# Performance work log

Measured on AMD Instinct MI355X. Metric: run time of the kernel, lower is better.

The kernel has to match this reference:

```python
import jax, jax.numpy as jnp
import numpy as np

B, C, H, W = 4, 64, 64, 64
K = C // 8  # conv_f / conv_g output channels (scale=8 since C>=8)


def setup_inputs() -> dict:
    key = jax.random.key(0)
    ks = jax.random.split(key, 8)
    x = jax.random.normal(ks[0], (B, C, H, W), dtype=jnp.float32)
    Wf = jax.random.normal(ks[1], (K, C), dtype=jnp.float32) * 0.05
    bf = jnp.zeros((K,), dtype=jnp.float32)
    Wg = jax.random.normal(ks[2], (K, C), dtype=jnp.float32) * 0.05
    bg = jnp.zeros((K,), dtype=jnp.float32)
    Wh = jax.random.normal(ks[3], (C, C), dtype=jnp.float32) * 0.05
    bh = jnp.zeros((C,), dtype=jnp.float32)
    gamma = jax.random.uniform(ks[4], (1,), dtype=jnp.float32)
    return {"x": x, "Wf": Wf, "bf": bf, "Wg": Wg, "bg": bg,
            "Wh": Wh, "bh": bh, "gamma": gamma}


def reference(x, Wf, bf, Wg, bg, Wh, bh, gamma):
    Bn, Cn, Hn, Wn = x.shape
    HW = Hn * Wn
    xf = x.reshape(Bn, Cn, HW)                               # [B, C, HW]
    # 1x1 convs == per-pixel linear maps over channels
    f = jnp.einsum('kc,bcn->bkn', Wf, xf) + bf[None, :, None]  # [B, K, HW]
    g = jnp.einsum('kc,bcn->bkn', Wg, xf) + bg[None, :, None]  # [B, K, HW]
    h = jnp.einsum('dc,bcn->bdn', Wh, xf) + bh[None, :, None]  # [B, C, HW]
    # s = f^T @ g  -> [B, HW, HW]
    s = jnp.einsum('bki,bkj->bij', f, g)
    # softmax over dim=1 (the first HW axis), matching F.softmax(s, dim=1)
    b = jax.nn.softmax(s, axis=1)
    # post-softmax lower-triangular mask applied to b^T (lower_tri=True)
    tri = jnp.tril(jnp.ones((HW, HW), dtype=x.dtype))
    b_masked = jnp.swapaxes(b, 1, 2) * tri                   # [B, HW, HW]
    o = jnp.einsum('bcn,bnm->bcm', h, b_masked)              # [B, C, HW]
    y = (gamma[0] * o + xf).reshape(Bn, Cn, Hn, Wn)
    return y
```

## Files before the change

### kernel.cpp

```cpp
#include <hip/hip_runtime.h>
#include <hip/hip_bf16.h>

#define HW 4096
#define CC 64
#define NB 4

typedef short bf16x8 __attribute__((ext_vector_type(8)));
typedef float f32x4 __attribute__((ext_vector_type(4)));

#define OFF_F  0
#define OFF_G  262144
#define OFF_H  524288
#define OFF_ZI 2621440
#define OFF_O  2686976

__device__ __forceinline__ float bf2f(short s) {
    unsigned u = ((unsigned)(unsigned short)s) << 16;
    return __uint_as_float(u);
}

__global__ __launch_bounds__(256) void k_prep(
    const float* __restrict__ x,
    const float* __restrict__ Wf, const float* __restrict__ bf,
    const float* __restrict__ Wg, const float* __restrict__ bg,
    const float* __restrict__ Wh, const float* __restrict__ bh,
    __hip_bfloat16* __restrict__ fb, __hip_bfloat16* __restrict__ gb,
    __hip_bfloat16* __restrict__ hb)
{
    __shared__ __align__(16) __hip_bfloat16 xT[64 * 72];
    __shared__ __align__(16) __hip_bfloat16 fgT[64 * 24];

    const int b  = blockIdx.y;
    const int n0 = blockIdx.x * 64;
    const int tid = (int)threadIdx.x;
    const int w = tid >> 6, lane = tid & 63, quad = lane >> 4, l15 = lane & 15;

    {
        const int n = lane;
        const float* xb = x + (size_t)b * (CC * HW) + n0 + n;
#pragma unroll
        for (int i = 0; i < 8; ++i) {
            const int c = (w + 4 * i) * 2;
            const float v0 = xb[(size_t)c * HW];
            const float v1 = xb[(size_t)(c + 1) * HW];
            __hip_bfloat16 t[2] = {__float2bfloat16(v0), __float2bfloat16(v1)};
            *reinterpret_cast<unsigned*>(&xT[n * 72 + c]) =
                *reinterpret_cast<const unsigned*>(t);
        }
    }

    bf16x8 wa[5][2];
#pragma unroll
    for (int mt = 0; mt < 5; ++mt) {
        const int row = mt * 16 + l15;
        const float* src = (row < 8) ? (Wf + row * 64)
                         : (row < 16) ? (Wg + (row - 8) * 64)
                                      : (Wh + (row - 16) * 64);
#pragma unroll
        for (int kk = 0; kk < 2; ++kk) {
            const float4 a = *(const float4*)(src + kk * 32 + quad * 8);
            const float4 c4 = *(const float4*)(src + kk * 32 + quad * 8 + 4);
            __hip_bfloat16 t[8];
            t[0] = __float2bfloat16(a.x);  t[1] = __float2bfloat16(a.y);
            t[2] = __float2bfloat16(a.z);  t[3] = __float2bfloat16(a.w);
            t[4] = __float2bfloat16(c4.x); t[5] = __float2bfloat16(c4.y);
            t[6] = __float2bfloat16(c4.z); t[7] = __float2bfloat16(c4.w);
            wa[mt][kk] = *reinterpret_cast<const bf16x8*>(t);
        }
    }

    f32x4 acc[5];
#pragma unroll
    for (int mt = 0; mt < 5; ++mt) {
#pragma unroll
        for (int r = 0; r < 4; ++r) {
            const int grow = mt * 16 + quad * 4 + r;
            acc[mt][r] = (grow < 8) ? bf[grow]
                       : (grow < 16) ? bg[grow - 8]
                                     : bh[grow - 16];
        }
    }

    __syncthreads();

    const bf16x8 b0 = *(const bf16x8*)&xT[(w * 16 + l15) * 72 + quad * 8];
    const bf16x8 b1 = *(const bf16x8*)&xT[(w * 16 + l15) * 72 + 32 + quad * 8];
#pragma unroll
    for (int mt = 0; mt < 5; ++mt) {
        acc[mt] = __builtin_amdgcn_mfma_f32_16x16x32_bf16(wa[mt][0], b0, acc[mt], 0, 0, 0);
        acc[mt] = __builtin_amdgcn_mfma_f32_16x16x32_bf16(wa[mt][1], b1, acc[mt], 0, 0, 0);
    }

#pragma unroll
    for (int mt = 1; mt < 5; ++mt) {
#pragma unroll
        for (int r = 0; r < 4; ++r) {
            const int hrow = (mt - 1) * 16 + quad * 4 + r;
            hb[((size_t)(b * 64 + hrow)) * HW + n0 + w * 16 + l15] =
                __float2bfloat16(acc[0 + mt][r]);
        }
    }

#pragma unroll
    for (int r = 0; r < 4; r += 2) {
        __hip_bfloat16 t[2] = {__float2bfloat16(acc[0][r]),
                               __float2bfloat16(acc[0][r + 1])};
        *reinterpret_cast<unsigned*>(&fgT[(w * 16 + l15) * 24 + quad * 4 + r]) =
            *reinterpret_cast<const unsigned*>(t);
    }
    __syncthreads();
    if (tid < 64) {
        const size_t bn = (size_t)b * HW + n0 + tid;
        *(float4*)(fb + bn * 8) = *(const float4*)&fgT[tid * 24];
    } else if (tid < 128) {
        const int n = tid - 64;
        const size_t bn = (size_t)b * HW + n0 + n;
        *(float4*)(gb + bn * 8) = *(const float4*)&fgT[n * 24 + 8];
    }
}

__global__ __launch_bounds__(256) void k_z(
    const __hip_bfloat16* __restrict__ fb, const __hip_bfloat16* __restrict__ gb,
    float* __restrict__ zinv)
{
    __shared__ __align__(16) __hip_bfloat16 fS[4096 * 8];
    __shared__ __align__(16) __hip_bfloat16 gS[64 * 8];
    __shared__ float zred[4][64];

    const int nt = blockIdx.x, b = blockIdx.y;
    const int n0 = nt * 64;
    const int tid = (int)threadIdx.x;
    const int w = tid >> 6, lane = tid & 63, quad = lane >> 4, l15 = lane & 15;

    const float4* fsrc = (const float4*)(fb + (size_t)b * HW * 8);
#pragma unroll
    for (int q = 0; q < 16; ++q)
        ((float4*)fS)[q * 256 + tid] = fsrc[q * 256 + tid];
    if (tid < 64)
        *(float4*)&gS[tid * 8] = *(const float4*)(gb + ((size_t)b * HW + n0 + tid) * 8);
    __syncthreads();

    const f32x4 cz = {0.f, 0.f, 0.f, 0.f};
    bf16x8 bgf[4];
#pragma unroll
    for (int ns = 0; ns < 4; ++ns) {
        bf16x8 v = {0, 0, 0, 0, 0, 0, 0, 0};
        if (quad == 0) v = *(const bf16x8*)&gS[(ns * 16 + l15) * 8];
        bgf[ns] = v;
    }

    float z[4] = {0.f, 0.f, 0.f, 0.f};
    for (int it = 0; it < 64; ++it) {
        const int i = it * 64 + w * 16;
        bf16x8 afr = {0, 0, 0, 0, 0, 0, 0, 0};
        if (quad == 0) afr = *(const bf16x8*)&fS[(i + l15) * 8];
#pragma unroll
        for (int ns = 0; ns < 4; ++ns) {
            f32x4 s = __builtin_amdgcn_mfma_f32_16x16x32_bf16(afr, bgf[ns], cz, 0, 0, 0);
            z[ns] += __expf(s[0]) + __expf(s[1]) + __expf(s[2]) + __expf(s[3]);
        }
    }

#pragma unroll
    for (int ns = 0; ns < 4; ++ns) {
        float v = z[ns];
        v += __shfl_xor(v, 16);
        v += __shfl_xor(v, 32);
        if (quad == 0) zred[w][ns * 16 + l15] = v;
    }
    __syncthreads();
    if (tid < 64) {
        float s = zred[0][tid] + zred[1][tid] + zred[2][tid] + zred[3][tid];
        zinv[(size_t)b * HW + n0 + tid] = 1.0f / s;
    }
}

__global__ __launch_bounds__(256) void k_attn(
    const __hip_bfloat16* __restrict__ fb, const __hip_bfloat16* __restrict__ gb,
    const __hip_bfloat16* __restrict__ hb, const float* __restrict__ zinv,
    __hip_bfloat16* __restrict__ opart)
{
    __shared__ __align__(16) __hip_bfloat16 gS[64 * 8];
    __shared__ __align__(16) float zS[64];
    __shared__ __align__(16) __hip_bfloat16 hT[64 * 72];
    __shared__ __align__(16) __hip_bfloat16 pT[64 * 72];

    const int hx = blockIdx.x;
    const int b  = blockIdx.y;
    const int r  = blockIdx.z;
    const int mt = (r < 32) ? r : 95 - r;
    const int m0 = mt * 64;
    const int tid = (int)threadIdx.x;
    const int w = tid >> 6, lane = tid & 63, quad = lane >> 4, l15 = lane & 15;

    const int c0s = tid >> 3,          ch0 = tid & 7;
    const int c1s = (256 + tid) >> 3,  ch1 = (256 + tid) & 7;

    const f32x4 cz = {0.f, 0.f, 0.f, 0.f};

    bf16x8 af = {0, 0, 0, 0, 0, 0, 0, 0};
    if (quad == 0)
        af = *(const bf16x8*)(fb + ((size_t)b * HW + m0 + w * 16 + l15) * 8);

    f32x4 accO[4];
#pragma unroll
    for (int i = 0; i < 4; ++i) accO[i] = cz;

    const int nc0 = mt + hx;
    float4 hv0 = make_float4(0.f, 0.f, 0.f, 0.f);
    float4 hv1 = hv0, gv = hv0, zv = hv0;
    if (nc0 < 64) {
        const int n0 = nc0 * 64;
        hv0 = *(const float4*)(hb + ((size_t)(b * 64 + c0s)) * HW + n0 + ch0 * 8);
        hv1 = *(const float4*)(hb + ((size_t)(b * 64 + c1s)) * HW + n0 + ch1 * 8);
        if (tid < 64)      gv = *(const float4*)(gb + ((size_t)b * HW + n0 + tid) * 8);
        else if (tid < 80) zv = *(const float4*)(zinv + (size_t)b * HW + n0 + (tid - 64) * 4);
    }

    for (int nc = nc0; nc < 64; nc += 4) {
        __syncthreads();
        *(float4*)&hT[c0s * 72 + ch0 * 8] = hv0;
        *(float4*)&hT[c1s * 72 + ch1 * 8] = hv1;
        if (tid < 64)      *(float4*)&gS[tid * 8] = gv;
        else if (tid < 80) *(float4*)&zS[(tid - 64) * 4] = zv;

        const int nn = nc + 4;
        if (nn < 64) {
            const int n1 = nn * 64;
            hv0 = *(const float4*)(hb + ((size_t)(b * 64 + c0s)) * HW + n1 + ch0 * 8);
            hv1 = *(const float4*)(hb + ((size_t)(b * 64 + c1s)) * HW + n1 + ch1 * 8);
            if (tid < 64)      gv = *(const float4*)(gb + ((size_t)b * HW + n1 + tid) * 8);
            else if (tid < 80) zv = *(const float4*)(zinv + (size_t)b * HW + n1 + (tid - 64) * 4);
        }
        __syncthreads();

        const int n0 = nc * 64;
        const bool diag = (nc == mt);
#pragma unroll
        for (int ns = 0; ns < 4; ++ns) {
            bf16x8 bg = {0, 0, 0, 0, 0, 0, 0, 0};
            if (quad == 0) bg = *(const bf16x8*)&gS[(ns * 16 + l15) * 8];
            f32x4 s = __builtin_amdgcn_mfma_f32_16x16x32_bf16(af, bg, cz, 0, 0, 0);
            const float zi = zS[ns * 16 + l15];
#pragma unroll
            for (int j = 0; j < 4; ++j) {
                float p = __expf(s[j]) * zi;
                if (diag) {
                    const int m = m0 + w * 16 + quad * 4 + j;
                    const int n = n0 + ns * 16 + l15;
                    if (n < m) p = 0.f;
                }
                pT[(w * 16 + quad * 4 + j) * 72 + ns * 16 + l15] = __float2bfloat16(p);
            }
        }
#pragma unroll
        for (int kb = 0; kb < 2; ++kb) {
            const bf16x8 ap =
                *(const bf16x8*)&pT[(w * 16 + l15) * 72 + kb * 32 + quad * 8];
#pragma unroll
            for (int cs = 0; cs < 4; ++cs) {
                const bf16x8 bh2 =
                    *(const bf16x8*)&hT[(cs * 16 + l15) * 72 + kb * 32 + quad * 8];
                accO[cs] = __builtin_amdgcn_mfma_f32_16x16x32_bf16(ap, bh2, accO[cs], 0, 0, 0);
            }
        }
    }

#pragma unroll
    for (int cs = 0; cs < 4; ++cs) {
        const int c = cs * 16 + l15;
        __hip_bfloat16 tmp[4];
#pragma unroll
        for (int j = 0; j < 4; ++j) tmp[j] = __float2bfloat16(accO[cs][j]);
        *(float2*)(opart + ((size_t)((hx * NB + b) * 64 + c)) * HW + m0 + w * 16 + quad * 4) =
            *(const float2*)tmp;
    }
}

__global__ __launch_bounds__(256) void k_epi(
    const __hip_bfloat16* __restrict__ opart, const float* __restrict__ x,
    const float* __restrict__ gamma, float* __restrict__ y)
{
    const int t = blockIdx.x * 256 + (int)threadIdx.x;
    const size_t e0 = (size_t)t * 8;
    const float ga = gamma[0];

    float acc[8] = {0, 0, 0, 0, 0, 0, 0, 0};
#pragma unroll
    for (int h = 0; h < 4; ++h) {
        const bf16x8 v = *(const bf16x8*)(opart + (size_t)h * (NB * CC * HW) + e0);
#pragma unroll
        for (int k = 0; k < 8; ++k) acc[k] += bf2f(v[k]);
    }
    const float4 x0 = *(const float4*)(x + e0);
    const float4 x1 = *(const float4*)(x + e0 + 4);
    float4 y0, y1;
    y0.x = ga * acc[0] + x0.x; y0.y = ga * acc[1] + x0.y;
    y0.z = ga * acc[2] + x0.z; y0.w = ga * acc[3] + x0.w;
    y1.x = ga * acc[4] + x1.x; y1.y = ga * acc[5] + x1.y;
    y1.z = ga * acc[6] + x1.z; y1.w = ga * acc[7] + x1.w;
    *(float4*)(y + e0) = y0;
    *(float4*)(y + e0 + 4) = y1;
}

extern "C" void kernel_launch(void* const* d_in, const int* in_sizes, int n_in,
                              void* d_out, int out_size, void* d_ws, size_t ws_size,
                              hipStream_t stream)
{
    const float* x     = (const float*)d_in[0];
    const float* Wf    = (const float*)d_in[1];
    const float* bf    = (const float*)d_in[2];
    const float* Wg    = (const float*)d_in[3];
    const float* bg    = (const float*)d_in[4];
    const float* Wh    = (const float*)d_in[5];
    const float* bh    = (const float*)d_in[6];
    const float* gamma = (const float*)d_in[7];

    char* ws = (char*)d_ws;
    __hip_bfloat16* fb = (__hip_bfloat16*)(ws + OFF_F);
    __hip_bfloat16* gb = (__hip_bfloat16*)(ws + OFF_G);
    __hip_bfloat16* hb = (__hip_bfloat16*)(ws + OFF_H);
    float* zinv = (float*)(ws + OFF_ZI);
    __hip_bfloat16* opart = (__hip_bfloat16*)(ws + OFF_O);
    float* y = (float*)d_out;

    k_prep<<<dim3(64, 4), 256, 0, stream>>>(x, Wf, bf, Wg, bg, Wh, bh, fb, gb, hb);
    k_z<<<dim3(64, 4), 256, 0, stream>>>(fb, gb, zinv);
    k_attn<<<dim3(4, 4, 64), 256, 0, stream>>>(fb, gb, hb, zinv, opart);
    k_epi<<<512, 256, 0, stream>>>(opart, x, gamma, y);
}
```

Measured before the change: 119.3 us.

## Split softmax denominator over i-chunks, fold log2e into f, vectorize P stores

The softmax denominator kernel now splits the 4096-long reduction into four chunks across a third grid dimension and writes partial sums; the attention kernel adds them and takes the reciprocal when staging each tile. log2(e) is folded into the f weights and bias so a raw exp2 instruction replaces expf. The score MFMA operands are swapped so each lane holds four consecutive n values, which allows one packed 8-byte store of P into shared memory. The aim is more parallelism and smaller LDS use in k_z, plus cheaper exponentials and fewer LDS writes in k_attn, at the cost of an extra partial-sum buffer.

```diff
diff --git a/kernel.cpp b/kernel.cpp
--- a/kernel.cpp
+++ b/kernel.cpp
@@ -11,13 +11,23 @@
 #define OFF_F  0
 #define OFF_G  262144
 #define OFF_H  524288
-#define OFF_ZI 2621440
-#define OFF_O  2686976
+#define OFF_ZP 2621440
+#define OFF_O  2883584
 
 __device__ __forceinline__ float bf2f(short s) {
     unsigned u = ((unsigned)(unsigned short)s) << 16;
     return __uint_as_float(u);
 }
+
+__device__ __forceinline__ float e2(float x) {
+#if __has_builtin(__builtin_amdgcn_exp2f)
+    return __builtin_amdgcn_exp2f(x);
+#else
+    return exp2f(x);
+#endif
+}
+
+#define LOG2E 1.44269504088896340736f
 
 __global__ __launch_bounds__(256) void k_prep(
     const float* __restrict__ x,
@@ -56,15 +66,16 @@
         const float* src = (row < 8) ? (Wf + row * 64)
                          : (row < 16) ? (Wg + (row - 8) * 64)
                                       : (Wh + (row - 16) * 64);
+        const float sc = (row < 8) ? LOG2E : 1.0f;
 #pragma unroll
         for (int kk = 0; kk < 2; ++kk) {
             const float4 a = *(const float4*)(src + kk * 32 + quad * 8);
             const float4 c4 = *(const float4*)(src + kk * 32 + quad * 8 + 4);
             __hip_bfloat16 t[8];
-            t[0] = __float2bfloat16(a.x);  t[1] = __float2bfloat16(a.y);
-            t[2] = __float2bfloat16(a.z);  t[3] = __float2bfloat16(a.w);
-            t[4] = __float2bfloat16(c4.x); t[5] = __float2bfloat16(c4.y);
-            t[6] = __float2bfloat16(c4.z); t[7] = __float2bfloat16(c4.w);
+            t[0] = __float2bfloat16(a.x * sc);  t[1] = __float2bfloat16(a.y * sc);
+            t[2] = __float2bfloat16(a.z * sc);  t[3] = __float2bfloat16(a.w * sc);
+            t[4] = __float2bfloat16(c4.x * sc); t[5] = __float2bfloat16(c4.y * sc);
+            t[6] = __float2bfloat16(c4.z * sc); t[7] = __float2bfloat16(c4.w * sc);
             wa[mt][kk] = *reinterpret_cast<const bf16x8*>(t);
         }
     }
@@ -75,7 +86,7 @@
 #pragma unroll
         for (int r = 0; r < 4; ++r) {
             const int grow = mt * 16 + quad * 4 + r;
-            acc[mt][r] = (grow < 8) ? bf[grow]
+            acc[mt][r] = (grow < 8) ? bf[grow] * LOG2E
                        : (grow < 16) ? bg[grow - 8]
                                      : bh[grow - 16];
         }
@@ -121,20 +132,20 @@
 
 __global__ __launch_bounds__(256) void k_z(
     const __hip_bfloat16* __restrict__ fb, const __hip_bfloat16* __restrict__ gb,
-    float* __restrict__ zinv)
-{
-    __shared__ __align__(16) __hip_bfloat16 fS[4096 * 8];
+    float* __restrict__ zpart)
+{
+    __shared__ __align__(16) __hip_bfloat16 fS[1024 * 8];
     __shared__ __align__(16) __hip_bfloat16 gS[64 * 8];
     __shared__ float zred[4][64];
 
-    const int nt = blockIdx.x, b = blockIdx.y;
-    const int n0 = nt * 64;
+    const int nt = blockIdx.x, b = blockIdx.y, is = blockIdx.z;
+    const int n0 = nt * 64, i0 = is * 1024;
     const int tid = (int)threadIdx.x;
     const int w = tid >> 6, lane = tid & 63, quad = lane >> 4, l15 = lane & 15;
 
-    const float4* fsrc = (const float4*)(fb + (size_t)b * HW * 8);
-#pragma unroll
-    for (int q = 0; q < 16; ++q)
+    const float4* fsrc = (const float4*)(fb + ((size_t)b * HW + i0) * 8);
+#pragma unroll
+    for (int q = 0; q < 4; ++q)
         ((float4*)fS)[q * 256 + tid] = fsrc[q * 256 + tid];
     if (tid < 64)
         *(float4*)&gS[tid * 8] = *(const float4*)(gb + ((size_t)b * HW + n0 + tid) * 8);
@@ -150,14 +161,14 @@
     }
 
     float z[4] = {0.f, 0.f, 0.f, 0.f};
-    for (int it = 0; it < 64; ++it) {
+    for (int it = 0; it < 16; ++it) {
         const int i = it * 64 + w * 16;
         bf16x8 afr = {0, 0, 0, 0, 0, 0, 0, 0};
         if (quad == 0) afr = *(const bf16x8*)&fS[(i + l15) * 8];
 #pragma unroll
         for (int ns = 0; ns < 4; ++ns) {
             f32x4 s = __builtin_amdgcn_mfma_f32_16x16x32_bf16(afr, bgf[ns], cz, 0, 0, 0);
-            z[ns] += __expf(s[0]) + __expf(s[1]) + __expf(s[2]) + __expf(s[3]);
+            z[ns] += e2(s[0]) + e2(s[1]) + e2(s[2]) + e2(s[3]);
         }
     }
 
@@ -170,14 +181,14 @@
     }
     __syncthreads();
     if (tid < 64) {
-        float s = zred[0][tid] + zred[1][tid] + zred[2][tid] + zred[3][tid];
-        zinv[(size_t)b * HW + n0 + tid] = 1.0f / s;
+        const float s = zred[0][tid] + zred[1][tid] + zred[2][tid] + zred[3][tid];
+        zpart[((size_t)b * HW + n0 + tid) * 4 + is] = s;
     }
 }
 
 __global__ __launch_bounds__(256) void k_attn(
     const __hip_bfloat16* __restrict__ fb, const __hip_bfloat16* __restrict__ gb,
-    const __hip_bfloat16* __restrict__ hb, const float* __restrict__ zinv,
+    const __hip_bfloat16* __restrict__ hb, const float* __restrict__ zpart,
     __hip_bfloat16* __restrict__ opart)
 {
     __shared__ __align__(16) __hip_bfloat16 gS[64 * 8];
@@ -213,24 +224,30 @@
         const int n0 = nc0 * 64;
         hv0 = *(const float4*)(hb + ((size_t)(b * 64 + c0s)) * HW + n0 + ch0 * 8);
         hv1 = *(const float4*)(hb + ((size_t)(b * 64 + c1s)) * HW + n0 + ch1 * 8);
-        if (tid < 64)      gv = *(const float4*)(gb + ((size_t)b * HW + n0 + tid) * 8);
-        else if (tid < 80) zv = *(const float4*)(zinv + (size_t)b * HW + n0 + (tid - 64) * 4);
+        if (tid < 64) {
+            gv = *(const float4*)(gb + ((size_t)b * HW + n0 + tid) * 8);
+            zv = *(const float4*)(zpart + ((size_t)b * HW + n0 + tid) * 4);
+        }
     }
 
     for (int nc = nc0; nc < 64; nc += 4) {
         __syncthreads();
         *(float4*)&hT[c0s * 72 + ch0 * 8] = hv0;
         *(float4*)&hT[c1s * 72 + ch1 * 8] = hv1;
-        if (tid < 64)      *(float4*)&gS[tid * 8] = gv;
-        else if (tid < 80) *(float4*)&zS[(tid - 64) * 4] = zv;
+        if (tid < 64) {
+            *(float4*)&gS[tid * 8] = gv;
+            zS[tid] = 1.0f / (zv.x + zv.y + zv.z + zv.w);
+        }
 
         const int nn = nc + 4;
         if (nn < 64) {
             const int n1 = nn * 64;
             hv0 = *(const float4*)(hb + ((size_t)(b * 64 + c0s)) * HW + n1 + ch0 * 8);
             hv1 = *(const float4*)(hb + ((size_t)(b * 64 + c1s)) * HW + n1 + ch1 * 8);
-            if (tid < 64)      gv = *(const float4*)(gb + ((size_t)b * HW + n1 + tid) * 8);
-            else if (tid < 80) zv = *(const float4*)(zinv + (size_t)b * HW + n1 + (tid - 64) * 4);
+            if (tid < 64) {
+                gv = *(const float4*)(gb + ((size_t)b * HW + n1 + tid) * 8);
+                zv = *(const float4*)(zpart + ((size_t)b * HW + n1 + tid) * 4);
+            }
         }
         __syncthreads();
 
@@ -238,20 +255,23 @@
         const bool diag = (nc == mt);
 #pragma unroll
         for (int ns = 0; ns < 4; ++ns) {
-            bf16x8 bg = {0, 0, 0, 0, 0, 0, 0, 0};
-            if (quad == 0) bg = *(const bf16x8*)&gS[(ns * 16 + l15) * 8];
-            f32x4 s = __builtin_amdgcn_mfma_f32_16x16x32_bf16(af, bg, cz, 0, 0, 0);
-            const float zi = zS[ns * 16 + l15];
+            bf16x8 ag = {0, 0, 0, 0, 0, 0, 0, 0};
+            if (quad == 0) ag = *(const bf16x8*)&gS[(ns * 16 + l15) * 8];
+            f32x4 s = __builtin_amdgcn_mfma_f32_16x16x32_bf16(ag, af, cz, 0, 0, 0);
+            const f32x4 ziv = *(const f32x4*)&zS[ns * 16 + quad * 4];
+            __hip_bfloat16 t[4];
 #pragma unroll
             for (int j = 0; j < 4; ++j) {
-                float p = __expf(s[j]) * zi;
+                float p = e2(s[j]) * ziv[j];
                 if (diag) {
-                    const int m = m0 + w * 16 + quad * 4 + j;
-                    const int n = n0 + ns * 16 + l15;
+                    const int n = n0 + ns * 16 + quad * 4 + j;
+                    const int m = m0 + w * 16 + l15;
                     if (n < m) p = 0.f;
                 }
-                pT[(w * 16 + quad * 4 + j) * 72 + ns * 16 + l15] = __float2bfloat16(p);
+                t[j] = __float2bfloat16(p);
             }
+            *(float2*)&pT[(w * 16 + l15) * 72 + ns * 16 + quad * 4] =
+                *(const float2*)t;
         }
 #pragma unroll
         for (int kb = 0; kb < 2; ++kb) {
@@ -320,12 +340,12 @@
     __hip_bfloat16* fb = (__hip_bfloat16*)(ws + OFF_F);
     __hip_bfloat16* gb = (__hip_bfloat16*)(ws + OFF_G);
     __hip_bfloat16* hb = (__hip_bfloat16*)(ws + OFF_H);
-    float* zinv = (float*)(ws + OFF_ZI);
+    float* zpart = (float*)(ws + OFF_ZP);
     __hip_bfloat16* opart = (__hip_bfloat16*)(ws + OFF_O);
     float* y = (float*)d_out;
 
     k_prep<<<dim3(64, 4), 256, 0, stream>>>(x, Wf, bf, Wg, bg, Wh, bh, fb, gb, hb);
-    k_z<<<dim3(64, 4), 256, 0, stream>>>(fb, gb, zinv);
-    k_attn<<<dim3(4, 4, 64), 256, 0, stream>>>(fb, gb, hb, zinv, opart);
+    k_z<<<dim3(64, 4, 4), 256, 0, stream>>>(fb, gb, zpart);
+    k_attn<<<dim3(4, 4, 64), 256, 0, stream>>>(fb, gb, hb, zpart, opart);
     k_epi<<<512, 256, 0, stream>>>(opart, x, gamma, y);
 }
```

After: 118.5 us. About the same (-0.7%).
